# Kernel tuning notes

Hardware: AMD Instinct MI355X
Metric: run time of the kernel (lower is better)

## Reference

```python
import jax, jax.numpy as jnp
import numpy as np

HEADS = 32


def _conv1x1(x, w, b):
    # x: (B, Cin, H, W); w: (Cout, Cin); 1x1 conv == per-pixel GEMM
    return jnp.einsum('bchw,oc->bohw', x, w) + b[None, :, None, None]


def _grid_sample2d_zeros(value, grid):
    # value: (N, C, H, W); grid: (N, H, W, 2), normalized coords in [-1, 1],
    # grid[..., 0] = x (width axis), grid[..., 1] = y (height axis).
    # Bilinear, align_corners=True, zeros padding applied per dimension.
    N, C, H, W = value.shape
    ix = (grid[..., 0] + 1.0) * (W - 1) * 0.5
    iy = (grid[..., 1] + 1.0) * (H - 1) * 0.5
    x0 = jnp.floor(ix)
    y0 = jnp.floor(iy)
    dx = ix - x0  # (N, H, W)
    dy = iy - y0
    x0i = x0.astype(jnp.int32)
    y0i = y0.astype(jnp.int32)
    x1i = x0i + 1
    y1i = y0i + 1

    def gather(yi, xi):
        valid = ((xi >= 0) & (xi < W) & (yi >= 0) & (yi < H))
        xc = jnp.clip(xi, 0, W - 1)
        yc = jnp.clip(yi, 0, H - 1)
        g = jax.vmap(lambda v, y, x: v[:, y, x])(value, yc, xc)  # (N, C, H, W)
        return g * valid[:, None, :, :].astype(value.dtype)

    out = (gather(y0i, x0i) * ((1.0 - dx) * (1.0 - dy))[:, None]
           + gather(y0i, x1i) * (dx * (1.0 - dy))[:, None]
           + gather(y1i, x0i) * ((1.0 - dx) * dy)[:, None]
           + gather(y1i, x1i) * (dx * dy)[:, None])
    return out


def _base_grid(H, W, dtype):
    ys = jnp.linspace(-1.0, 1.0, H, dtype=dtype)
    xs = jnp.linspace(-1.0, 1.0, W, dtype=dtype)
    gy, gx = jnp.meshgrid(ys, xs, indexing='ij')
    return jnp.stack([gx, gy], axis=-1)  # (H, W, 2)


def setup_inputs() -> dict:
    key = jax.random.key(0)
    k = jax.random.split(key, 8)
    B, Cin, Cout, H, W = 4, 256, 256, 128, 128
    u = jax.random.normal(k[0], (B, Cin, H, W), dtype=jnp.float32)
    s_in = 1.0 / np.sqrt(Cin)
    s_out = 1.0 / np.sqrt(Cout)
    w1 = jax.random.normal(k[1], (Cout, Cin), dtype=jnp.float32) * s_in
    b1 = jax.random.normal(k[2], (Cout,), dtype=jnp.float32) * 0.01
    w2 = jax.random.normal(k[3], (2 * HEADS, Cout), dtype=jnp.float32) * (0.1 * s_out)
    b2 = jax.random.normal(k[4], (2 * HEADS,), dtype=jnp.float32) * 0.01
    wv = jax.random.normal(k[5], (Cout, Cin), dtype=jnp.float32) * s_in
    bv = jax.random.normal(k[6], (Cout,), dtype=jnp.float32) * 0.01
    return {"u": u, "w1": w1, "b1": b1, "w2": w2, "b2": b2, "wv": wv, "bv": bv}


def reference(u, w1, b1, w2, b2, wv, bv):
    B, Cin, H, W = u.shape
    # flow_head: 1x1 conv -> ReLU -> 1x1 conv producing n_dims*heads channels
    h = jax.nn.relu(_conv1x1(u, w1, b1))
    flow = _conv1x1(h, w2, b2)          # (B, heads*2, H, W)
    value = _conv1x1(u, wv, bv)         # (B, Cout, H, W)
    Ci = value.shape[1] // HEADS
    # 'B (heads dir) H W -> (B heads) H W dir'
    flow = flow.reshape(B, HEADS, 2, H, W).transpose(0, 1, 3, 4, 2)
    flow = flow.reshape(B * HEADS, H, W, 2)
    # 'B (heads C_i) H W -> (B heads) C_i H W'
    value = value.reshape(B * HEADS, Ci, H, W)
    grid = _base_grid(H, W, u.dtype)[None] + flow  # (B*heads, H, W, 2)
    warp = _grid_sample2d_zeros(value, grid)       # (B*heads, Ci, H, W)
    # '(B heads) C_i H W -> B (heads C_i) H W'
    return warp.reshape(B, HEADS * Ci, H, W)
```

## Files before the change

### kernel.cpp

```cpp
#include <hip/hip_runtime.h>
#include <cstddef>

#define HW 16384

typedef short s8v __attribute__((ext_vector_type(8)));
typedef short s4v __attribute__((ext_vector_type(4)));
typedef float f4v __attribute__((ext_vector_type(4)));

__device__ inline short f2b(float x) {
    union { float f; unsigned u; } v; v.f = x;
    unsigned r = v.u + 0x7fff + ((v.u >> 16) & 1);
    return (short)(r >> 16);
}
__device__ inline float b2f(short h) {
    union { unsigned u; float f; } v;
    v.u = ((unsigned)(unsigned short)h) << 16;
    return v.f;
}

__global__ __launch_bounds__(256) void k_prep_w(
    const float* __restrict__ w1, const float* __restrict__ wv,
    const float* __restrict__ w2,
    short* __restrict__ Wthi, short* __restrict__ Wtlo,
    short* __restrict__ w2thi, short* __restrict__ w2tlo)
{
    int tid = blockIdx.x * 256 + threadIdx.x;
    if (tid < 131072) {
        int c = tid >> 14, r = tid & 16383, ch = r >> 5, kk = r & 31;
        float f = (ch < 256) ? w1[ch * 256 + c * 32 + kk]
                             : wv[(ch - 256) * 256 + c * 32 + kk];
        short hi = f2b(f);
        Wthi[tid] = hi;
        if (ch < 256) Wtlo[(c * 256 + ch) * 32 + kk] = f2b(f - b2f(hi));
    } else {
        int o = tid - 131072;
        int c = o >> 11, r = o & 2047, dir = r >> 5, kk = r & 31;
        float f = w2[dir * 256 + c * 32 + kk];
        short hi = f2b(f);
        w2thi[o] = hi;
        w2tlo[o] = f2b(f - b2f(hi));
    }
}

__global__ __launch_bounds__(256, 2) void k_mega(
    const float* __restrict__ u,
    const short* __restrict__ Wthi, const short* __restrict__ Wtlo,
    const short* __restrict__ w2thi, const short* __restrict__ w2tlo,
    const float* __restrict__ b1, const float* __restrict__ bv,
    const float* __restrict__ b2,
    unsigned short* __restrict__ vbuf, float* __restrict__ flow)
{
    __shared__ __attribute__((aligned(16))) char smem[69632];
    short* T1h = (short*)smem;
    short* T1l = T1h + 4352;
    short* T2h = (short*)(smem + 17408);
    short* T2l = T2h + 4608;
    short* vt  = (short*)smem;
    short* hhi = (short*)smem;
    short* hlo = (short*)(smem + 34816);

    const int t = threadIdx.x;
    const int l = t & 63;
    const int w = t >> 6;
    const int lr = l & 15;
    const int quad = l >> 4;
    const int quad8 = quad * 8;
    const int pt = blockIdx.x * 64;
    const int b  = pt >> 14;
    const int p0 = pt & 16383;
    const float* ub = u + (size_t)b * 256 * HW + p0;
    const int pxB = 16 * w + lr;

    f4v acc_h[4][4], acc_v[4][4];
    #pragma unroll
    for (int i = 0; i < 4; ++i)
        #pragma unroll
        for (int j = 0; j < 4; ++j) {
            acc_h[i][j] = (f4v){0.f, 0.f, 0.f, 0.f};
            acc_v[i][j] = (f4v){0.f, 0.f, 0.f, 0.f};
        }

    float4 cur[4];
    #pragma unroll
    for (int i = 0; i < 4; ++i) {
        int idx = t + 256 * i;
        int ch = idx >> 4, px4 = (idx & 15) * 4;
        cur[i] = *reinterpret_cast<const float4*>(ub + (size_t)ch * HW + px4);
    }

    for (int pair = 0; pair < 4; ++pair) {
        #pragma unroll
        for (int i = 0; i < 4; ++i) {
            int idx = t + 256 * i;
            int ch = idx >> 4, px4 = (idx & 15) * 4;
            float4 v = cur[i];
            short h0 = f2b(v.x), h1 = f2b(v.y), h2 = f2b(v.z), h3 = f2b(v.w);
            s4v hv = {h0, h1, h2, h3};
            s4v lv = {f2b(v.x - b2f(h0)), f2b(v.y - b2f(h1)),
                      f2b(v.z - b2f(h2)), f2b(v.w - b2f(h3))};
            *reinterpret_cast<s4v*>(T1h + ch * 68 + px4) = hv;
            *reinterpret_cast<s4v*>(T1l + ch * 68 + px4) = lv;
        }
        __syncthreads();
        #pragma unroll
        for (int part = 0; part < 2; ++part) {
            const short* src = part ? T1l : T1h;
            short* dst = part ? T2l : T2h;
            #pragma unroll
            for (int j = 0; j < 4; ++j) {
                int k4 = (l >> 4) + 4 * j;
                s4v v = { src[(4 * k4 + 0) * 68 + pxB],
                          src[(4 * k4 + 1) * 68 + pxB],
                          src[(4 * k4 + 2) * 68 + pxB],
                          src[(4 * k4 + 3) * 68 + pxB] };
                *reinterpret_cast<s4v*>(dst + pxB * 72 + 4 * k4) = v;
            }
        }
        __syncthreads();
        if (pair < 3) {
            #pragma unroll
            for (int i = 0; i < 4; ++i) {
                int idx = t + 256 * i;
                int ch = idx >> 4, px4 = (idx & 15) * 4;
                cur[i] = *reinterpret_cast<const float4*>(
                    ub + (size_t)((pair + 1) * 64 + ch) * HW + px4);
            }
        }
        #pragma unroll
        for (int s = 0; s < 2; ++s) {
            int c = pair * 2 + s;
            s8v bh4[4], bl4[4];
            #pragma unroll
            for (int j = 0; j < 4; ++j) {
                bh4[j] = *reinterpret_cast<const s8v*>(T2h + (16 * j + lr) * 72 + s * 32 + quad8);
                bl4[j] = *reinterpret_cast<const s8v*>(T2l + (16 * j + lr) * 72 + s * 32 + quad8);
            }
            #pragma unroll
            for (int i = 0; i < 4; ++i) {
                const size_t wb = ((size_t)c * 512 + 64 * w + 16 * i + lr) * 32 + quad8;
                s8v ahi = *reinterpret_cast<const s8v*>(Wthi + wb);
                s8v av  = *reinterpret_cast<const s8v*>(Wthi + wb + 256 * 32);
                s8v alo = *reinterpret_cast<const s8v*>(
                    Wtlo + ((size_t)c * 256 + 64 * w + 16 * i + lr) * 32 + quad8);
                #pragma unroll
                for (int j = 0; j < 4; ++j) {
                    acc_h[i][j] = __builtin_amdgcn_mfma_f32_16x16x32_bf16(ahi, bh4[j], acc_h[i][j], 0, 0, 0);
                    acc_h[i][j] = __builtin_amdgcn_mfma_f32_16x16x32_bf16(ahi, bl4[j], acc_h[i][j], 0, 0, 0);
                    acc_h[i][j] = __builtin_amdgcn_mfma_f32_16x16x32_bf16(alo, bh4[j], acc_h[i][j], 0, 0, 0);
                    acc_v[i][j] = __builtin_amdgcn_mfma_f32_16x16x32_bf16(av,  bh4[j], acc_v[i][j], 0, 0, 0);
                }
            }
        }
        __syncthreads();
    }

    #pragma unroll
    for (int i = 0; i < 4; ++i) {
        float4 bias = *reinterpret_cast<const float4*>(bv + 64 * w + 16 * i + 4 * quad);
        #pragma unroll
        for (int j = 0; j < 4; ++j) {
            int px = 16 * j + lr;
            s4v pk = { f2b(acc_v[i][j][0] + bias.x), f2b(acc_v[i][j][1] + bias.y),
                       f2b(acc_v[i][j][2] + bias.z), f2b(acc_v[i][j][3] + bias.w) };
            *reinterpret_cast<s4v*>(vt + px * 272 + 64 * w + 16 * i + 4 * quad) = pk;
        }
    }
    __syncthreads();
    {
        int px = t >> 2, ch0 = (t & 3) * 64;
        size_t pixg = (size_t)(b << 14) + p0 + px;
        #pragma unroll
        for (int e = 0; e < 8; ++e) {
            s8v vv = *reinterpret_cast<const s8v*>(vt + px * 272 + ch0 + 8 * e);
            *reinterpret_cast<s8v*>(vbuf + pixg * 256 + ch0 + 8 * e) = vv;
        }
    }
    __syncthreads();

    #pragma unroll
    for (int i = 0; i < 4; ++i) {
        float4 bias = *reinterpret_cast<const float4*>(b1 + 64 * w + 16 * i + 4 * quad);
        #pragma unroll
        for (int j = 0; j < 4; ++j) {
            int px = 16 * j + lr;
            float v0 = fmaxf(acc_h[i][j][0] + bias.x, 0.f);
            float v1 = fmaxf(acc_h[i][j][1] + bias.y, 0.f);
            float v2 = fmaxf(acc_h[i][j][2] + bias.z, 0.f);
            float v3 = fmaxf(acc_h[i][j][3] + bias.w, 0.f);
            short h0 = f2b(v0), h1 = f2b(v1), h2 = f2b(v2), h3 = f2b(v3);
            s4v hv = {h0, h1, h2, h3};
            s4v lv = {f2b(v0 - b2f(h0)), f2b(v1 - b2f(h1)),
                      f2b(v2 - b2f(h2)), f2b(v3 - b2f(h3))};
            int chb = 64 * w + 16 * i + 4 * quad;
            *reinterpret_cast<s4v*>(hhi + px * 272 + chb) = hv;
            *reinterpret_cast<s4v*>(hlo + px * 272 + chb) = lv;
        }
    }
    __syncthreads();

    f4v acc_f[4];
    #pragma unroll
    for (int j = 0; j < 4; ++j) acc_f[j] = (f4v){0.f, 0.f, 0.f, 0.f};
    #pragma unroll
    for (int c = 0; c < 8; ++c) {
        const size_t wb = ((size_t)c * 64 + 16 * w + lr) * 32 + quad8;
        s8v ahi = *reinterpret_cast<const s8v*>(w2thi + wb);
        s8v alo = *reinterpret_cast<const s8v*>(w2tlo + wb);
        #pragma unroll
        for (int j = 0; j < 4; ++j) {
            int px = 16 * j + lr;
            s8v bhh = *reinterpret_cast<const s8v*>(hhi + px * 272 + c * 32 + quad8);
            s8v bll = *reinterpret_cast<const s8v*>(hlo + px * 272 + c * 32 + quad8);
            acc_f[j] = __builtin_amdgcn_mfma_f32_16x16x32_bf16(ahi, bhh, acc_f[j], 0, 0, 0);
            acc_f[j] = __builtin_amdgcn_mfma_f32_16x16x32_bf16(ahi, bll, acc_f[j], 0, 0, 0);
            acc_f[j] = __builtin_amdgcn_mfma_f32_16x16x32_bf16(alo, bhh, acc_f[j], 0, 0, 0);
        }
    }
    float4 b2v = *reinterpret_cast<const float4*>(b2 + 16 * w + 4 * quad);
    #pragma unroll
    for (int r = 0; r < 4; ++r) {
        int dir = 16 * w + 4 * quad + r;
        float bias = (r == 0) ? b2v.x : (r == 1) ? b2v.y : (r == 2) ? b2v.z : b2v.w;
        #pragma unroll
        for (int j = 0; j < 4; ++j)
            flow[((size_t)b * 64 + dir) * HW + p0 + 16 * j + lr] = acc_f[j][r] + bias;
    }
}

__global__ __launch_bounds__(256) void k_warp(
    const float* __restrict__ flow, const unsigned short* __restrict__ vbuf,
    float* __restrict__ out)
{
    const int g = blockIdx.x * 256 + threadIdx.x;
    const int p = g & 16383;
    const int n = g >> 14;
    const int b = n >> 5;
    const int head = n & 31;
    const int y = p >> 7;
    const int x = p & 127;

    float fx = flow[((size_t)b * 64 + 2 * head + 0) * HW + p];
    float fy = flow[((size_t)b * 64 + 2 * head + 1) * HW + p];
    float ix = (float)x + fx * 63.5f;
    float iy = (float)y + fy * 63.5f;

    float x0f = floorf(ix), y0f = floorf(iy);
    float dx = ix - x0f, dy = iy - y0f;
    int x0 = (int)x0f, y0 = (int)y0f;
    int x1 = x0 + 1,   y1 = y0 + 1;

    bool vx0 = (x0 >= 0) & (x0 < 128);
    bool vx1 = (x1 >= 0) & (x1 < 128);
    bool vy0 = (y0 >= 0) & (y0 < 128);
    bool vy1 = (y1 >= 0) & (y1 < 128);
    int x0c = min(max(x0, 0), 127), x1c = min(max(x1, 0), 127);
    int y0c = min(max(y0, 0), 127), y1c = min(max(y1, 0), 127);

    float w00 = (1.f - dx) * (1.f - dy) * ((vx0 & vy0) ? 1.f : 0.f);
    float w10 = dx * (1.f - dy)        * ((vx1 & vy0) ? 1.f : 0.f);
    float w01 = (1.f - dx) * dy        * ((vx0 & vy1) ? 1.f : 0.f);
    float w11 = dx * dy                * ((vx1 & vy1) ? 1.f : 0.f);

    const unsigned short* vb = vbuf + ((size_t)(b << 14)) * 256 + head * 8;
    s8v v00 = *reinterpret_cast<const s8v*>(vb + (size_t)(y0c * 128 + x0c) * 256);
    s8v v10 = *reinterpret_cast<const s8v*>(vb + (size_t)(y0c * 128 + x1c) * 256);
    s8v v01 = *reinterpret_cast<const s8v*>(vb + (size_t)(y1c * 128 + x0c) * 256);
    s8v v11 = *reinterpret_cast<const s8v*>(vb + (size_t)(y1c * 128 + x1c) * 256);

    float* ob = out + ((size_t)b * 256 + head * 8) * HW + p;
    #pragma unroll
    for (int ci = 0; ci < 8; ++ci) {
        float v = w00 * b2f(v00[ci]) + w10 * b2f(v10[ci])
                + w01 * b2f(v01[ci]) + w11 * b2f(v11[ci]);
        ob[(size_t)ci * HW] = v;
    }
}

extern "C" void kernel_launch(void* const* d_in, const int* in_sizes, int n_in,
                              void* d_out, int out_size, void* d_ws, size_t ws_size,
                              hipStream_t stream) {
    const float* u  = (const float*)d_in[0];
    const float* w1 = (const float*)d_in[1];
    const float* b1 = (const float*)d_in[2];
    const float* w2 = (const float*)d_in[3];
    const float* b2 = (const float*)d_in[4];
    const float* wv = (const float*)d_in[5];
    const float* bv = (const float*)d_in[6];

    char* ws = (char*)d_ws;
    unsigned short* vbuf = (unsigned short*)ws;
    float* flow  = (float*)(ws + 33554432ull);
    short* Wthi  = (short*)(ws + 50331648ull);
    short* Wtlo  = Wthi + 131072;
    short* w2thi = Wtlo + 65536;
    short* w2tlo = w2thi + 16384;
    float* out = (float*)d_out;

    k_prep_w<<<dim3(576),  dim3(256), 0, stream>>>(w1, wv, w2, Wthi, Wtlo, w2thi, w2tlo);
    k_mega  <<<dim3(1024), dim3(256), 0, stream>>>(u, Wthi, Wtlo, w2thi, w2tlo,
                                                   b1, bv, b2, vbuf, flow);
    k_warp  <<<dim3(8192), dim3(256), 0, stream>>>(flow, vbuf, out);
}
```

Baseline: 217.9 us.

## Double mega-kernel threads, head-major value buffer, XCD-aware warp scheduling

Launches the fused GEMM kernel with 512 threads per block, so each wave covers half as many output channels, which spreads the MFMA work across more waves. Plain __syncthreads calls are replaced by an explicit lgkmcnt wait plus s_barrier. The value buffer moves from pixel-major to head-major layout, so each warp head's bilinear gathers touch a compact 256KB region. The warp kernel remaps block IDs so each XCD handles contiguous heads, which should improve L2 locality. Low-bf16 residuals are also truncated instead of rounded, saving a few ALU ops at a small cost in accuracy.

```diff
diff --git a/kernel.cpp b/kernel.cpp
--- a/kernel.cpp
+++ b/kernel.cpp
@@ -12,10 +12,18 @@
     unsigned r = v.u + 0x7fff + ((v.u >> 16) & 1);
     return (short)(r >> 16);
 }
+__device__ inline short f2bt(float x) {
+    union { float f; unsigned u; } v; v.f = x;
+    return (short)(v.u >> 16);
+}
 __device__ inline float b2f(short h) {
     union { unsigned u; float f; } v;
     v.u = ((unsigned)(unsigned short)h) << 16;
     return v.f;
+}
+
+__device__ inline void bar_lgkm() {
+    asm volatile("s_waitcnt lgkmcnt(0)\n\ts_barrier" ::: "memory");
 }
 
 __global__ __launch_bounds__(256) void k_prep_w(
@@ -42,7 +50,7 @@
     }
 }
 
-__global__ __launch_bounds__(256, 2) void k_mega(
+__global__ __launch_bounds__(512, 4) void k_mega(
     const float* __restrict__ u,
     const short* __restrict__ Wthi, const short* __restrict__ Wtlo,
     const short* __restrict__ w2thi, const short* __restrict__ w2tlo,
@@ -69,63 +77,64 @@
     const int b  = pt >> 14;
     const int p0 = pt & 16383;
     const float* ub = u + (size_t)b * 256 * HW + p0;
-    const int pxB = 16 * w + lr;
-
-    f4v acc_h[4][4], acc_v[4][4];
-    #pragma unroll
-    for (int i = 0; i < 4; ++i)
+
+    f4v acc_h[2][4], acc_v[2][4];
+    #pragma unroll
+    for (int i = 0; i < 2; ++i)
         #pragma unroll
         for (int j = 0; j < 4; ++j) {
             acc_h[i][j] = (f4v){0.f, 0.f, 0.f, 0.f};
             acc_v[i][j] = (f4v){0.f, 0.f, 0.f, 0.f};
         }
 
-    float4 cur[4];
-    #pragma unroll
-    for (int i = 0; i < 4; ++i) {
-        int idx = t + 256 * i;
-        int ch = idx >> 4, px4 = (idx & 15) * 4;
-        cur[i] = *reinterpret_cast<const float4*>(ub + (size_t)ch * HW + px4);
-    }
-
-    for (int pair = 0; pair < 4; ++pair) {
-        #pragma unroll
-        for (int i = 0; i < 4; ++i) {
-            int idx = t + 256 * i;
+    float4 cur[2];
+    auto loadU = [&](int pr) {
+        #pragma unroll
+        for (int i = 0; i < 2; ++i) {
+            int idx = t + 512 * i;
+            int ch = idx >> 4, px4 = (idx & 15) * 4;
+            cur[i] = *reinterpret_cast<const float4*>(
+                ub + (size_t)(pr * 64 + ch) * HW + px4);
+        }
+    };
+    auto stageA = [&]() {
+        #pragma unroll
+        for (int i = 0; i < 2; ++i) {
+            int idx = t + 512 * i;
             int ch = idx >> 4, px4 = (idx & 15) * 4;
             float4 v = cur[i];
             short h0 = f2b(v.x), h1 = f2b(v.y), h2 = f2b(v.z), h3 = f2b(v.w);
             s4v hv = {h0, h1, h2, h3};
-            s4v lv = {f2b(v.x - b2f(h0)), f2b(v.y - b2f(h1)),
-                      f2b(v.z - b2f(h2)), f2b(v.w - b2f(h3))};
+            s4v lv = {f2bt(v.x - b2f(h0)), f2bt(v.y - b2f(h1)),
+                      f2bt(v.z - b2f(h2)), f2bt(v.w - b2f(h3))};
             *reinterpret_cast<s4v*>(T1h + ch * 68 + px4) = hv;
             *reinterpret_cast<s4v*>(T1l + ch * 68 + px4) = lv;
         }
-        __syncthreads();
+    };
+    auto stageB = [&]() {
         #pragma unroll
         for (int part = 0; part < 2; ++part) {
             const short* src = part ? T1l : T1h;
             short* dst = part ? T2l : T2h;
             #pragma unroll
-            for (int j = 0; j < 4; ++j) {
-                int k4 = (l >> 4) + 4 * j;
-                s4v v = { src[(4 * k4 + 0) * 68 + pxB],
-                          src[(4 * k4 + 1) * 68 + pxB],
-                          src[(4 * k4 + 2) * 68 + pxB],
-                          src[(4 * k4 + 3) * 68 + pxB] };
-                *reinterpret_cast<s4v*>(dst + pxB * 72 + 4 * k4) = v;
+            for (int j = 0; j < 2; ++j) {
+                int k4 = w + 8 * j;
+                s4v v = { src[(4 * k4 + 0) * 68 + l],
+                          src[(4 * k4 + 1) * 68 + l],
+                          src[(4 * k4 + 2) * 68 + l],
+                          src[(4 * k4 + 3) * 68 + l] };
+                *reinterpret_cast<s4v*>(dst + l * 72 + 4 * k4) = v;
             }
         }
-        __syncthreads();
-        if (pair < 3) {
-            #pragma unroll
-            for (int i = 0; i < 4; ++i) {
-                int idx = t + 256 * i;
-                int ch = idx >> 4, px4 = (idx & 15) * 4;
-                cur[i] = *reinterpret_cast<const float4*>(
-                    ub + (size_t)((pair + 1) * 64 + ch) * HW + px4);
-            }
-        }
+    };
+
+    loadU(0);
+    for (int pair = 0; pair < 4; ++pair) {
+        stageA();
+        bar_lgkm();
+        stageB();
+        bar_lgkm();
+        if (pair < 3) loadU(pair + 1);
         #pragma unroll
         for (int s = 0; s < 2; ++s) {
             int c = pair * 2 + s;
@@ -136,12 +145,12 @@
                 bl4[j] = *reinterpret_cast<const s8v*>(T2l + (16 * j + lr) * 72 + s * 32 + quad8);
             }
             #pragma unroll
-            for (int i = 0; i < 4; ++i) {
-                const size_t wb = ((size_t)c * 512 + 64 * w + 16 * i + lr) * 32 + quad8;
+            for (int i = 0; i < 2; ++i) {
+                const size_t wb = ((size_t)c * 512 + 32 * w + 16 * i + lr) * 32 + quad8;
                 s8v ahi = *reinterpret_cast<const s8v*>(Wthi + wb);
                 s8v av  = *reinterpret_cast<const s8v*>(Wthi + wb + 256 * 32);
                 s8v alo = *reinterpret_cast<const s8v*>(
-                    Wtlo + ((size_t)c * 256 + 64 * w + 16 * i + lr) * 32 + quad8);
+                    Wtlo + ((size_t)c * 256 + 32 * w + 16 * i + lr) * 32 + quad8);
                 #pragma unroll
                 for (int j = 0; j < 4; ++j) {
                     acc_h[i][j] = __builtin_amdgcn_mfma_f32_16x16x32_bf16(ahi, bh4[j], acc_h[i][j], 0, 0, 0);
@@ -151,35 +160,38 @@
                 }
             }
         }
-        __syncthreads();
-    }
-
-    #pragma unroll
-    for (int i = 0; i < 4; ++i) {
-        float4 bias = *reinterpret_cast<const float4*>(bv + 64 * w + 16 * i + 4 * quad);
+        bar_lgkm();
+    }
+
+    #pragma unroll
+    for (int i = 0; i < 2; ++i) {
+        float4 bias = *reinterpret_cast<const float4*>(bv + 32 * w + 16 * i + 4 * quad);
         #pragma unroll
         for (int j = 0; j < 4; ++j) {
             int px = 16 * j + lr;
             s4v pk = { f2b(acc_v[i][j][0] + bias.x), f2b(acc_v[i][j][1] + bias.y),
                        f2b(acc_v[i][j][2] + bias.z), f2b(acc_v[i][j][3] + bias.w) };
-            *reinterpret_cast<s4v*>(vt + px * 272 + 64 * w + 16 * i + 4 * quad) = pk;
-        }
-    }
-    __syncthreads();
+            *reinterpret_cast<s4v*>(vt + px * 272 + 32 * w + 16 * i + 4 * quad) = pk;
+        }
+    }
+    bar_lgkm();
     {
-        int px = t >> 2, ch0 = (t & 3) * 64;
-        size_t pixg = (size_t)(b << 14) + p0 + px;
-        #pragma unroll
-        for (int e = 0; e < 8; ++e) {
-            s8v vv = *reinterpret_cast<const s8v*>(vt + px * 272 + ch0 + 8 * e);
-            *reinterpret_cast<s8v*>(vbuf + pixg * 256 + ch0 + 8 * e) = vv;
-        }
-    }
-    __syncthreads();
-
-    #pragma unroll
-    for (int i = 0; i < 4; ++i) {
-        float4 bias = *reinterpret_cast<const float4*>(b1 + 64 * w + 16 * i + 4 * quad);
+        int px = t >> 3;
+        int hg = t & 7;
+        size_t pix = (size_t)p0 + px;
+        #pragma unroll
+        for (int e = 0; e < 4; ++e) {
+            int hh = hg + 8 * e;
+            s8v vv = *reinterpret_cast<const s8v*>(vt + px * 272 + hh * 8);
+            *reinterpret_cast<s8v*>(
+                vbuf + ((((size_t)(b * 32 + hh)) << 14) + pix) * 8) = vv;
+        }
+    }
+    bar_lgkm();
+
+    #pragma unroll
+    for (int i = 0; i < 2; ++i) {
+        float4 bias = *reinterpret_cast<const float4*>(b1 + 32 * w + 16 * i + 4 * quad);
         #pragma unroll
         for (int j = 0; j < 4; ++j) {
             int px = 16 * j + lr;
@@ -189,26 +201,28 @@
             float v3 = fmaxf(acc_h[i][j][3] + bias.w, 0.f);
             short h0 = f2b(v0), h1 = f2b(v1), h2 = f2b(v2), h3 = f2b(v3);
             s4v hv = {h0, h1, h2, h3};
-            s4v lv = {f2b(v0 - b2f(h0)), f2b(v1 - b2f(h1)),
-                      f2b(v2 - b2f(h2)), f2b(v3 - b2f(h3))};
-            int chb = 64 * w + 16 * i + 4 * quad;
+            s4v lv = {f2bt(v0 - b2f(h0)), f2bt(v1 - b2f(h1)),
+                      f2bt(v2 - b2f(h2)), f2bt(v3 - b2f(h3))};
+            int chb = 32 * w + 16 * i + 4 * quad;
             *reinterpret_cast<s4v*>(hhi + px * 272 + chb) = hv;
             *reinterpret_cast<s4v*>(hlo + px * 272 + chb) = lv;
         }
     }
-    __syncthreads();
-
-    f4v acc_f[4];
-    #pragma unroll
-    for (int j = 0; j < 4; ++j) acc_f[j] = (f4v){0.f, 0.f, 0.f, 0.f};
+    bar_lgkm();
+
+    const int dg = w & 3;
+    const int ph = w >> 2;
+    f4v acc_f[2];
+    #pragma unroll
+    for (int j = 0; j < 2; ++j) acc_f[j] = (f4v){0.f, 0.f, 0.f, 0.f};
     #pragma unroll
     for (int c = 0; c < 8; ++c) {
-        const size_t wb = ((size_t)c * 64 + 16 * w + lr) * 32 + quad8;
+        const size_t wb = ((size_t)c * 64 + 16 * dg + lr) * 32 + quad8;
         s8v ahi = *reinterpret_cast<const s8v*>(w2thi + wb);
         s8v alo = *reinterpret_cast<const s8v*>(w2tlo + wb);
         #pragma unroll
-        for (int j = 0; j < 4; ++j) {
-            int px = 16 * j + lr;
+        for (int j = 0; j < 2; ++j) {
+            int px = 32 * ph + 16 * j + lr;
             s8v bhh = *reinterpret_cast<const s8v*>(hhi + px * 272 + c * 32 + quad8);
             s8v bll = *reinterpret_cast<const s8v*>(hlo + px * 272 + c * 32 + quad8);
             acc_f[j] = __builtin_amdgcn_mfma_f32_16x16x32_bf16(ahi, bhh, acc_f[j], 0, 0, 0);
@@ -216,14 +230,14 @@
             acc_f[j] = __builtin_amdgcn_mfma_f32_16x16x32_bf16(alo, bhh, acc_f[j], 0, 0, 0);
         }
     }
-    float4 b2v = *reinterpret_cast<const float4*>(b2 + 16 * w + 4 * quad);
+    float4 b2v = *reinterpret_cast<const float4*>(b2 + 16 * dg + 4 * quad);
     #pragma unroll
     for (int r = 0; r < 4; ++r) {
-        int dir = 16 * w + 4 * quad + r;
+        int dir = 16 * dg + 4 * quad + r;
         float bias = (r == 0) ? b2v.x : (r == 1) ? b2v.y : (r == 2) ? b2v.z : b2v.w;
         #pragma unroll
-        for (int j = 0; j < 4; ++j)
-            flow[((size_t)b * 64 + dir) * HW + p0 + 16 * j + lr] = acc_f[j][r] + bias;
+        for (int j = 0; j < 2; ++j)
+            flow[((size_t)b * 64 + dir) * HW + p0 + 32 * ph + 16 * j + lr] = acc_f[j][r] + bias;
     }
 }
 
@@ -231,9 +245,11 @@
     const float* __restrict__ flow, const unsigned short* __restrict__ vbuf,
     float* __restrict__ out)
 {
-    const int g = blockIdx.x * 256 + threadIdx.x;
-    const int p = g & 16383;
-    const int n = g >> 14;
+    const int bid = blockIdx.x;
+    const int xcd = bid & 7;
+    const int k   = bid >> 3;
+    const int n   = xcd * 16 + (k >> 6);
+    const int p   = ((k & 63) << 8) + threadIdx.x;
     const int b = n >> 5;
     const int head = n & 31;
     const int y = p >> 7;
@@ -261,11 +277,11 @@
     float w01 = (1.f - dx) * dy        * ((vx0 & vy1) ? 1.f : 0.f);
     float w11 = dx * dy                * ((vx1 & vy1) ? 1.f : 0.f);
 
-    const unsigned short* vb = vbuf + ((size_t)(b << 14)) * 256 + head * 8;
-    s8v v00 = *reinterpret_cast<const s8v*>(vb + (size_t)(y0c * 128 + x0c) * 256);
-    s8v v10 = *reinterpret_cast<const s8v*>(vb + (size_t)(y0c * 128 + x1c) * 256);
-    s8v v01 = *reinterpret_cast<const s8v*>(vb + (size_t)(y1c * 128 + x0c) * 256);
-    s8v v11 = *reinterpret_cast<const s8v*>(vb + (size_t)(y1c * 128 + x1c) * 256);
+    const unsigned short* vb = vbuf + (((size_t)n) << 14) * 8;
+    s8v v00 = *reinterpret_cast<const s8v*>(vb + (size_t)(y0c * 128 + x0c) * 8);
+    s8v v10 = *reinterpret_cast<const s8v*>(vb + (size_t)(y0c * 128 + x1c) * 8);
+    s8v v01 = *reinterpret_cast<const s8v*>(vb + (size_t)(y1c * 128 + x0c) * 8);
+    s8v v11 = *reinterpret_cast<const s8v*>(vb + (size_t)(y1c * 128 + x1c) * 8);
 
     float* ob = out + ((size_t)b * 256 + head * 8) * HW + p;
     #pragma unroll
@@ -297,7 +313,7 @@
     float* out = (float*)d_out;
 
     k_prep_w<<<dim3(576),  dim3(256), 0, stream>>>(w1, wv, w2, Wthi, Wtlo, w2thi, w2tlo);
-    k_mega  <<<dim3(1024), dim3(256), 0, stream>>>(u, Wthi, Wtlo, w2thi, w2tlo,
+    k_mega  <<<dim3(1024), dim3(512), 0, stream>>>(u, Wthi, Wtlo, w2thi, w2tlo,
                                                    b1, bv, b2, vbuf, flow);
     k_warp  <<<dim3(8192), dim3(256), 0, stream>>>(flow, vbuf, out);
 }
```

Measured after the change: 234.2 us. +7.5%, slower.
